# Optimization experiments

Hardware: AMD Instinct MI355X
Metric: run time of the kernel (lower is better)

The kernel has to match this reference:

```python
import jax, jax.numpy as jnp
import numpy as np

B, S, H = 4, 4096, 2880
E, K = 32, 4


def setup_inputs() -> dict:
    key = jax.random.key(0)
    k1, k2 = jax.random.split(key)
    hidden_states = jax.random.normal(k1, (B, S, H), dtype=jnp.float32)
    # router weight, scaled like a typical init (std ~ 1/sqrt(H))
    weight = jax.random.normal(k2, (E, H), dtype=jnp.float32) / np.sqrt(H)
    bias = jnp.zeros((E,), dtype=jnp.float32)
    return {"hidden_states": hidden_states, "weight": weight, "bias": bias}


def reference(hidden_states, weight, bias):
    b, s, h = hidden_states.shape
    x = hidden_states.reshape(-1, h)                     # [T, H]
    logits = jnp.einsum('th,eh->te', x, weight) + bias   # [T, E]
    # select top-k logits (sorted descending), then softmax over the subset
    topk_logits, topk_idx = jax.lax.top_k(logits, K)     # [T, K]
    topk_weight = jax.nn.softmax(topk_logits.astype(jnp.float32), axis=-1)
    return topk_idx, topk_weight
```

## Files before the change

kernel.cpp:

```cpp
#include <hip/hip_runtime.h>
#include <math.h>

#define H_DIM 2880
#define E_NUM 32
#define TOPK 4
#define TT 32
#define KW 64
#define NSTG 45
#define WSTRIDE 512
#define WBUF 2048
#define REDR 36
#define LGTO 4608
#define SMSZ 5760

#define GLD16(gp, lp)                                                  \
    __builtin_amdgcn_global_load_lds(                                  \
        (const __attribute__((address_space(1))) void*)(gp),           \
        (__attribute__((address_space(3))) void*)(lp), 16, 0, 0)

__global__ __attribute__((amdgpu_flat_work_group_size(256, 256),
                          amdgpu_waves_per_eu(2, 2))) void gate_fused(
    const float* __restrict__ x, const float* __restrict__ w,
    const float* __restrict__ bias, float* __restrict__ out, int T) {
    __shared__ float sm[SMSZ];
    const int tid = threadIdx.x;
    const int lane = tid & 63;
    const int wq = __builtin_amdgcn_readfirstlane(tid >> 6);
    const int tt = lane & 3;
    const int et = (lane >> 2) & 3;
    const int ksl = lane >> 4;
    const int t0 = blockIdx.x * TT;
    const int ksd = wq * 16 + ksl * 4;

    const int d0 = lane * 4, d1 = 256 + lane * 4;
    const float* gw0 = w + (size_t)(wq * 8 + d0 / KW) * H_DIM + (d0 % KW);
    const float* gw1 = w + (size_t)(wq * 8 + d1 / KW) * H_DIM + (d1 % KW);
    const int lw0 = wq * WSTRIDE + d0;
    const int lw1 = wq * WSTRIDE + d1;

    const float* xb = x + (size_t)t0 * H_DIM;
    int xo0 = (tt * 8 + 0) * H_DIM + ksd, xo1 = (tt * 8 + 1) * H_DIM + ksd;
    int xo2 = (tt * 8 + 2) * H_DIM + ksd, xo3 = (tt * 8 + 3) * H_DIM + ksd;
    int xo4 = (tt * 8 + 4) * H_DIM + ksd, xo5 = (tt * 8 + 5) * H_DIM + ksd;
    int xo6 = (tt * 8 + 6) * H_DIM + ksd, xo7 = (tt * 8 + 7) * H_DIM + ksd;

    float4 a0l = make_float4(0.f, 0.f, 0.f, 0.f), a0h = a0l, a1l = a0l, a1h = a0l;
    float4 a2l = a0l, a2h = a0l, a3l = a0l, a3h = a0l;
    float4 a4l = a0l, a4h = a0l, a5l = a0l, a5h = a0l;
    float4 a6l = a0l, a6h = a0l, a7l = a0l, a7h = a0l;
    float4 xq0, xq1, xq2, xq3, xq4, xq5, xq6, xq7, wA, wB;

    GLD16(gw0, &sm[lw0]); GLD16(gw1, &sm[lw1]);
    gw0 += KW; gw1 += KW;
    xq0 = *(const float4*)(xb + xo0); xq1 = *(const float4*)(xb + xo1);
    xq2 = *(const float4*)(xb + xo2); xq3 = *(const float4*)(xb + xo3);
    xq4 = *(const float4*)(xb + xo4); xq5 = *(const float4*)(xb + xo5);
    xq6 = *(const float4*)(xb + xo6); xq7 = *(const float4*)(xb + xo7);

#define DOT(XQ, WQ) (XQ.x * WQ.x + XQ.y * WQ.y + XQ.z * WQ.z + XQ.w * WQ.w)
#define FMAE(AL, AH, WQ)                                               \
    do {                                                               \
        AL.x += DOT(xq0, WQ); AL.y += DOT(xq1, WQ);                    \
        AL.z += DOT(xq2, WQ); AL.w += DOT(xq3, WQ);                    \
        AH.x += DOT(xq4, WQ); AH.y += DOT(xq5, WQ);                    \
        AH.z += DOT(xq6, WQ); AH.w += DOT(xq7, WQ);                    \
    } while (0)

#pragma unroll 1
    for (int s = 0; s < NSTG; ++s) {
        asm volatile("s_waitcnt vmcnt(0)" ::: "memory");
        __builtin_amdgcn_s_barrier();
        asm volatile("" ::: "memory");

        if (s + 1 < NSTG) {
            const int pn = (s + 1) & 1;
            GLD16(gw0, &sm[lw0 + pn * WBUF]);
            GLD16(gw1, &sm[lw1 + pn * WBUF]);
            gw0 += KW; gw1 += KW;
        }

        const float* wp = &sm[(s & 1) * WBUF + et * (8 * KW) + ksd];
        wA = *(const float4*)(wp + 0 * KW);
        wB = *(const float4*)(wp + 1 * KW); FMAE(a0l, a0h, wA);
        wA = *(const float4*)(wp + 2 * KW); FMAE(a1l, a1h, wB);
        wB = *(const float4*)(wp + 3 * KW); FMAE(a2l, a2h, wA);
        wA = *(const float4*)(wp + 4 * KW); FMAE(a3l, a3h, wB);
        wB = *(const float4*)(wp + 5 * KW); FMAE(a4l, a4h, wA);
        wA = *(const float4*)(wp + 6 * KW); FMAE(a5l, a5h, wB);
        wB = *(const float4*)(wp + 7 * KW); FMAE(a6l, a6h, wA);
        FMAE(a7l, a7h, wB);

        if (s + 1 < NSTG) {
            xo0 += KW; xo1 += KW; xo2 += KW; xo3 += KW;
            xo4 += KW; xo5 += KW; xo6 += KW; xo7 += KW;
            xq0 = *(const float4*)(xb + xo0); xq1 = *(const float4*)(xb + xo1);
            xq2 = *(const float4*)(xb + xo2); xq3 = *(const float4*)(xb + xo3);
            xq4 = *(const float4*)(xb + xo4); xq5 = *(const float4*)(xb + xo5);
            xq6 = *(const float4*)(xb + xo6); xq7 = *(const float4*)(xb + xo7);
        }
    }

    __syncthreads();

#define FOLD4(V)                                        \
    do {                                                \
        V.x += __shfl_xor(V.x, 16, 64); V.x += __shfl_xor(V.x, 32, 64); \
        V.y += __shfl_xor(V.y, 16, 64); V.y += __shfl_xor(V.y, 32, 64); \
        V.z += __shfl_xor(V.z, 16, 64); V.z += __shfl_xor(V.z, 32, 64); \
        V.w += __shfl_xor(V.w, 16, 64); V.w += __shfl_xor(V.w, 32, 64); \
    } while (0)
    FOLD4(a0l); FOLD4(a0h); FOLD4(a1l); FOLD4(a1h);
    FOLD4(a2l); FOLD4(a2h); FOLD4(a3l); FOLD4(a3h);
    FOLD4(a4l); FOLD4(a4h); FOLD4(a5l); FOLD4(a5h);
    FOLD4(a6l); FOLD4(a6h); FOLD4(a7l); FOLD4(a7h);

    if (ksl == 0) {
#define STROW(I, HF, CP)                                                     \
    do {                                                                     \
        float* rp = &sm[wq * (TT * REDR) + (tt * 8 + I) * REDR + et * 8];    \
        *(float4*)(rp + 0) =                                                 \
            make_float4(a0##HF.CP, a1##HF.CP, a2##HF.CP, a3##HF.CP);         \
        *(float4*)(rp + 4) =                                                 \
            make_float4(a4##HF.CP, a5##HF.CP, a6##HF.CP, a7##HF.CP);         \
    } while (0)
        STROW(0, l, x); STROW(1, l, y); STROW(2, l, z); STROW(3, l, w);
        STROW(4, h, x); STROW(5, h, y); STROW(6, h, z); STROW(7, h, w);
    }
    __syncthreads();

    {
        const int tok = tid >> 3, e4 = (tid & 7) * 4;
        float4 sg = *(const float4*)(bias + e4);
#pragma unroll
        for (int q = 0; q < 4; ++q) {
            float4 v = *(const float4*)&sm[q * (TT * REDR) + tok * REDR + e4];
            sg.x += v.x; sg.y += v.y; sg.z += v.z; sg.w += v.w;
        }
        *(float4*)&sm[LGTO + tok * REDR + e4] = sg;
    }
    __syncthreads();

    if (tid < TT) {
        const int t = t0 + tid;
        float logit[E_NUM];
#pragma unroll
        for (int j = 0; j < 8; ++j) {
            float4 v = *(const float4*)&sm[LGTO + tid * REDR + j * 4];
            logit[j * 4] = v.x; logit[j * 4 + 1] = v.y;
            logit[j * 4 + 2] = v.z; logit[j * 4 + 3] = v.w;
        }

        int idx[TOPK];
        float val[TOPK];
#pragma unroll
        for (int k = 0; k < TOPK; ++k) {
            float best = -INFINITY;
            int bi = 0;
#pragma unroll
            for (int e = 0; e < E_NUM; ++e) {
                bool taken = false;
                for (int p2 = 0; p2 < k; ++p2) taken = taken || (idx[p2] == e);
                float v = logit[e];
                if (!taken && v > best) { best = v; bi = e; }
            }
            idx[k] = bi;
            val[k] = best;
        }
        float ex[TOPK], ssum = 0.f;
#pragma unroll
        for (int k = 0; k < TOPK; ++k) { ex[k] = expf(val[k] - val[0]); ssum += ex[k]; }
        const float inv = 1.f / ssum;

        *(float4*)(out + (size_t)t * 4) =
            make_float4((float)idx[0], (float)idx[1], (float)idx[2], (float)idx[3]);
        *(float4*)(out + (size_t)T * 4 + (size_t)t * 4) =
            make_float4(ex[0] * inv, ex[1] * inv, ex[2] * inv, ex[3] * inv);
    }
}

extern "C" void kernel_launch(void* const* d_in, const int* in_sizes, int n_in,
                              void* d_out, int out_size, void* d_ws, size_t ws_size,
                              hipStream_t stream) {
    const float* x    = (const float*)d_in[0];
    const float* w    = (const float*)d_in[1];
    const float* bias = (const float*)d_in[2];
    float* out = (float*)d_out;

    const int T = in_sizes[0] / H_DIM;

    gate_fused<<<dim3(T / TT), 256, 0, stream>>>(x, w, bias, out, T);
}
```

Baseline: 317.2 us.

## Triple-buffer activation register prefetch with partial vmcnt waits

Replaces the single set of activation registers with three rotating float4 register sets, so the x loads for stage s+2 are in flight while stage s computes. The loop is manually unrolled by three, with an explicit tail for the last stages. The full vmcnt(0) wait becomes vmcnt(8), which waits only for the weight global-to-LDS copy and older x loads and leaves the newest x loads outstanding. The goal is to hide global memory latency on the streaming activation reads. The cost is roughly 64 more VGPRs and ordering that depends on a precise count of outstanding loads.

After: 608.4 us. 1.92x slower.

```diff
diff --git a/kernel.cpp b/kernel.cpp
--- a/kernel.cpp
+++ b/kernel.cpp
@@ -38,7 +38,7 @@
     const int lw0 = wq * WSTRIDE + d0;
     const int lw1 = wq * WSTRIDE + d1;
 
-    const float* xb = x + (size_t)t0 * H_DIM;
+    const float* xbase = x + (size_t)t0 * H_DIM;
     int xo0 = (tt * 8 + 0) * H_DIM + ksd, xo1 = (tt * 8 + 1) * H_DIM + ksd;
     int xo2 = (tt * 8 + 2) * H_DIM + ksd, xo3 = (tt * 8 + 3) * H_DIM + ksd;
     int xo4 = (tt * 8 + 4) * H_DIM + ksd, xo5 = (tt * 8 + 5) * H_DIM + ksd;
@@ -48,62 +48,102 @@
     float4 a2l = a0l, a2h = a0l, a3l = a0l, a3h = a0l;
     float4 a4l = a0l, a4h = a0l, a5l = a0l, a5h = a0l;
     float4 a6l = a0l, a6h = a0l, a7l = a0l, a7h = a0l;
-    float4 xq0, xq1, xq2, xq3, xq4, xq5, xq6, xq7, wA, wB;
-
+    float4 va0, va1, va2, va3, va4, va5, va6, va7;
+    float4 vb0, vb1, vb2, vb3, vb4, vb5, vb6, vb7;
+    float4 vc0, vc1, vc2, vc3, vc4, vc5, vc6, vc7;
+    float4 wA, wB;
+
+#define SEQ asm volatile("" ::: "memory")
+#define WAIT8 asm volatile("s_waitcnt vmcnt(8)" ::: "memory")
+#define WAIT0 asm volatile("s_waitcnt vmcnt(0)" ::: "memory")
+#define BARX                                   \
+    do {                                       \
+        __builtin_amdgcn_s_barrier();          \
+        asm volatile("" ::: "memory");         \
+    } while (0)
+#define INCX                                                        \
+    do {                                                            \
+        xo0 += KW; xo1 += KW; xo2 += KW; xo3 += KW;                 \
+        xo4 += KW; xo5 += KW; xo6 += KW; xo7 += KW;                 \
+    } while (0)
+#define LOADX(P)                                                    \
+    do {                                                            \
+        P##0 = *(const float4*)(xbase + xo0);                       \
+        P##1 = *(const float4*)(xbase + xo1);                       \
+        P##2 = *(const float4*)(xbase + xo2);                       \
+        P##3 = *(const float4*)(xbase + xo3);                       \
+        P##4 = *(const float4*)(xbase + xo4);                       \
+        P##5 = *(const float4*)(xbase + xo5);                       \
+        P##6 = *(const float4*)(xbase + xo6);                       \
+        P##7 = *(const float4*)(xbase + xo7);                       \
+    } while (0)
+#define DOT(XQ, WQ) (XQ.x * WQ.x + XQ.y * WQ.y + XQ.z * WQ.z + XQ.w * WQ.w)
+#define FMAE(AL, AH, WQ, P)                                         \
+    do {                                                            \
+        AL.x += DOT(P##0, WQ); AL.y += DOT(P##1, WQ);               \
+        AL.z += DOT(P##2, WQ); AL.w += DOT(P##3, WQ);               \
+        AH.x += DOT(P##4, WQ); AH.y += DOT(P##5, WQ);               \
+        AH.z += DOT(P##6, WQ); AH.w += DOT(P##7, WQ);               \
+    } while (0)
+#define COMPUTE(P, PAR)                                             \
+    do {                                                            \
+        const float* wp = &sm[(PAR) * WBUF + et * (8 * KW) + ksd];  \
+        wA = *(const float4*)(wp + 0 * KW);                         \
+        wB = *(const float4*)(wp + 1 * KW); FMAE(a0l, a0h, wA, P);  \
+        wA = *(const float4*)(wp + 2 * KW); FMAE(a1l, a1h, wB, P);  \
+        wB = *(const float4*)(wp + 3 * KW); FMAE(a2l, a2h, wA, P);  \
+        wA = *(const float4*)(wp + 4 * KW); FMAE(a3l, a3h, wB, P);  \
+        wB = *(const float4*)(wp + 5 * KW); FMAE(a4l, a4h, wA, P);  \
+        wA = *(const float4*)(wp + 6 * KW); FMAE(a5l, a5h, wB, P);  \
+        wB = *(const float4*)(wp + 7 * KW); FMAE(a6l, a6h, wA, P);  \
+        FMAE(a7l, a7h, wB, P);                                      \
+    } while (0)
+#define STAGE(PCUR, PNXT, PAR)                                      \
+    do {                                                            \
+        WAIT8;                                                      \
+        BARX;                                                       \
+        GLD16(gw0, &sm[lw0 + (1 - (PAR)) * WBUF]);                  \
+        GLD16(gw1, &sm[lw1 + (1 - (PAR)) * WBUF]);                  \
+        gw0 += KW; gw1 += KW;                                       \
+        SEQ;                                                        \
+        INCX;                                                       \
+        LOADX(PNXT);                                                \
+        SEQ;                                                        \
+        COMPUTE(PCUR, PAR);                                         \
+    } while (0)
+
+    LOADX(va);
+    SEQ;
     GLD16(gw0, &sm[lw0]); GLD16(gw1, &sm[lw1]);
     gw0 += KW; gw1 += KW;
-    xq0 = *(const float4*)(xb + xo0); xq1 = *(const float4*)(xb + xo1);
-    xq2 = *(const float4*)(xb + xo2); xq3 = *(const float4*)(xb + xo3);
-    xq4 = *(const float4*)(xb + xo4); xq5 = *(const float4*)(xb + xo5);
-    xq6 = *(const float4*)(xb + xo6); xq7 = *(const float4*)(xb + xo7);
-
-#define DOT(XQ, WQ) (XQ.x * WQ.x + XQ.y * WQ.y + XQ.z * WQ.z + XQ.w * WQ.w)
-#define FMAE(AL, AH, WQ)                                               \
-    do {                                                               \
-        AL.x += DOT(xq0, WQ); AL.y += DOT(xq1, WQ);                    \
-        AL.z += DOT(xq2, WQ); AL.w += DOT(xq3, WQ);                    \
-        AH.x += DOT(xq4, WQ); AH.y += DOT(xq5, WQ);                    \
-        AH.z += DOT(xq6, WQ); AH.w += DOT(xq7, WQ);                    \
-    } while (0)
+    SEQ;
+    INCX;
+    LOADX(vb);
+    SEQ;
 
 #pragma unroll 1
-    for (int s = 0; s < NSTG; ++s) {
-        asm volatile("s_waitcnt vmcnt(0)" ::: "memory");
-        __builtin_amdgcn_s_barrier();
-        asm volatile("" ::: "memory");
-
-        if (s + 1 < NSTG) {
-            const int pn = (s + 1) & 1;
-            GLD16(gw0, &sm[lw0 + pn * WBUF]);
-            GLD16(gw1, &sm[lw1 + pn * WBUF]);
-            gw0 += KW; gw1 += KW;
-        }
-
-        const float* wp = &sm[(s & 1) * WBUF + et * (8 * KW) + ksd];
-        wA = *(const float4*)(wp + 0 * KW);
-        wB = *(const float4*)(wp + 1 * KW); FMAE(a0l, a0h, wA);
-        wA = *(const float4*)(wp + 2 * KW); FMAE(a1l, a1h, wB);
-        wB = *(const float4*)(wp + 3 * KW); FMAE(a2l, a2h, wA);
-        wA = *(const float4*)(wp + 4 * KW); FMAE(a3l, a3h, wB);
-        wB = *(const float4*)(wp + 5 * KW); FMAE(a4l, a4h, wA);
-        wA = *(const float4*)(wp + 6 * KW); FMAE(a5l, a5h, wB);
-        wB = *(const float4*)(wp + 7 * KW); FMAE(a6l, a6h, wA);
-        FMAE(a7l, a7h, wB);
-
-        if (s + 1 < NSTG) {
-            xo0 += KW; xo1 += KW; xo2 += KW; xo3 += KW;
-            xo4 += KW; xo5 += KW; xo6 += KW; xo7 += KW;
-            xq0 = *(const float4*)(xb + xo0); xq1 = *(const float4*)(xb + xo1);
-            xq2 = *(const float4*)(xb + xo2); xq3 = *(const float4*)(xb + xo3);
-            xq4 = *(const float4*)(xb + xo4); xq5 = *(const float4*)(xb + xo5);
-            xq6 = *(const float4*)(xb + xo6); xq7 = *(const float4*)(xb + xo7);
-        }
-    }
+    for (int it = 0; it < 14; ++it) {
+        const int p0 = it & 1, p1 = p0 ^ 1;
+        STAGE(va, vc, p0);
+        STAGE(vb, va, p1);
+        STAGE(vc, vb, p0);
+    }
+    WAIT8; BARX;
+    GLD16(gw0, &sm[lw0 + WBUF]); GLD16(gw1, &sm[lw1 + WBUF]);
+    gw0 += KW; gw1 += KW;
+    SEQ; INCX; LOADX(vc); SEQ;
+    COMPUTE(va, 0);
+    WAIT8; BARX;
+    GLD16(gw0, &sm[lw0]); GLD16(gw1, &sm[lw1]);
+    SEQ;
+    COMPUTE(vb, 1);
+    WAIT0; BARX;
+    COMPUTE(vc, 0);
 
     __syncthreads();
 
-#define FOLD4(V)                                        \
-    do {                                                \
+#define FOLD4(V)                                                        \
+    do {                                                                \
         V.x += __shfl_xor(V.x, 16, 64); V.x += __shfl_xor(V.x, 32, 64); \
         V.y += __shfl_xor(V.y, 16, 64); V.y += __shfl_xor(V.y, 32, 64); \
         V.z += __shfl_xor(V.z, 16, 64); V.z += __shfl_xor(V.z, 32, 64); \
```
